# Optimization experiments

Hardware: AMD Instinct MI355X
Metric: run time of the kernel (lower is better)

Reference implementation:

```python
import jax, jax.numpy as jnp
import numpy as np
import math

# ---- constants derived from PCF.__init__(nbbins=50, sigma=0.25, npoints=1024, n_rmax=5) ----
NBBINS = 50
SIGMA = 0.25
NPOINTS = 1024
N_RMAX = 5
RMAX = float(2.0 * np.sqrt(1.0 / (2.0 * np.sqrt(3.0) * NPOINTS)))
_STEP = N_RMAX / NBBINS
RS = np.array([(i + 1) * _STEP * RMAX for i in range(NBBINS)], dtype=np.float32)
AREA = np.array([math.pi * ((r + 0.5 * RMAX) ** 2 - max(0.0, r - 0.5 * RMAX) ** 2) for r in RS],
                dtype=np.float32)
GF = float(1.0 / (np.sqrt(math.pi) * SIGMA))


def _gaussian_kernel(x):
    return GF * jnp.exp(-(x * x) / (SIGMA * SIGMA))


def _perimeter_weight(x, y, rs):
    """x, y: [N] disk centers in [0,1]^2; rs: [B]. Returns [N, B] inverse in-domain perimeter fraction."""
    full = jnp.full((x.shape[0], rs.shape[0]), 2.0 * math.pi, dtype=x.dtype)

    def corr(full_angle, dx, dy):
        # dx, dy: [N] distance to a domain edge (as in the four blocks of perimeter_weight)
        mask = rs[None, :] > dx[:, None]                       # [N, B]
        alpha = jnp.arccos(jnp.clip(dx[:, None] / rs[None, :], -1.0, 1.0))
        sub = (jnp.minimum(alpha, jnp.arctan2(dy, dx)[:, None])
               + jnp.minimum(alpha, jnp.arctan2(1.0 - dy, dx)[:, None]))
        return full_angle - jnp.where(mask, sub, 0.0)

    full = corr(full, x, y)          # left edge
    full = corr(full, 1.0 - x, y)    # right edge
    full = corr(full, y, x)          # bottom edge
    full = corr(full, 1.0 - y, x)    # top edge
    peri = jnp.clip(full / (2.0 * math.pi), 0.0, 1.0)
    pos = peri > 0
    return jnp.where(pos, 1.0 / jnp.where(pos, peri, 1.0), 0.0)


def _disk_distance(pa, pb, rmax):
    """pa: [Na,3], pb: [Nb,3] disks (x, y, r) -> pairwise disk distance [Na, Nb] (repo utils.diskDistance)."""
    diff = pa[:, None, 0:2] - pb[None, :, 0:2]
    d = jnp.sqrt(jnp.sum(diff * diff, axis=-1))                # [Na, Nb]
    ra = pa[:, 2][:, None]
    rb = pb[None, :, 2]
    r1 = jnp.maximum(ra, rb)
    r2 = jnp.minimum(ra, rb)
    extent = jnp.maximum(d + r1 + r2, 2.0 * r1)
    overlap = jnp.clip(r1 + r2 - d, 0.0, None)
    return (extent - overlap + d + r1 - r2) / rmax


def _pcf_forward(disks_a, disks_b, same_category):
    rs = jnp.asarray(RS)
    area = jnp.asarray(AREA)
    na = disks_a.shape[0]
    nb = disks_b.shape[0]
    dist = _disk_distance(disks_a, disks_b, RMAX)              # [Na, Nb]
    # val[i, j, b] = gauss(rs_b / rmax - dist_ij)
    val = _gaussian_kernel(rs[None, None, :] / RMAX - dist[:, :, None])  # [Na, Nb, B]
    if same_category:
        # exclude self-pair j == i (torch.cat of slices around i)
        eye = jnp.eye(na, nb, dtype=val.dtype)
        val = val * (1.0 - eye)[:, :, None]
    contrib = jnp.sum(val, axis=1)                             # [Na, B]
    weights = _perimeter_weight(disks_a[:, 0], disks_a[:, 1], rs)  # [Na, B] (diskfact = 1/domainLength = 1)
    density = contrib * weights / area[None, :] / nb           # [Na, B]
    pcf_mean = jnp.sum(density, axis=0) / na                   # [B]
    pcf_lower = jnp.min(density, axis=0)
    pcf_upper = jnp.max(density, axis=0)
    pcf = jnp.stack([rs / RMAX, pcf_mean], axis=1)             # [B, 2]
    return pcf, pcf_lower, pcf_upper


def setup_inputs() -> dict:
    key = jax.random.key(0)
    ka, kb = jax.random.split(key)
    disks_a = jax.random.uniform(ka, (1024, 3), dtype=jnp.float32)
    disks_b = jax.random.uniform(kb, (1024, 3), dtype=jnp.float32)
    return {"disks_a": disks_a, "disks_b": disks_b, "same_category": 0}


def reference(disks_a, disks_b, same_category):
    return _pcf_forward(disks_a, disks_b, same_category)
```

## Files before the change

### kernel.cpp

```cpp
#include <hip/hip_runtime.h>
#include <math.h>

#define NB 50

__device__ __forceinline__ float dev_rmax() {
    return (float)(2.0 * sqrt(1.0 / (2.0 * sqrt(3.0) * 1024.0)));
}

__global__ void __launch_bounds__(64)
pcf_density_kernel(const float* __restrict__ da, const float* __restrict__ db,
                   const int* __restrict__ scp, float* __restrict__ dens,
                   int na, int nb)
{
    const float RMAX = dev_rmax();
    const float inv_rmax = 1.0f / RMAX;
    const int i   = blockIdx.x;
    const int tid = threadIdx.x;
    const int sc  = scp[0];

    const float ax = da[3*i+0];
    const float ay = da[3*i+1];
    const float ar = da[3*i+2];

    float acc[NB];
#pragma unroll
    for (int b = 0; b < NB; ++b) acc[b] = 0.0f;

    for (int j = tid; j < nb; j += 64) {
        const float bx = db[3*j+0];
        const float by = db[3*j+1];
        const float br = db[3*j+2];
        const float dx = ax - bx;
        const float dy = ay - by;
        const float d  = sqrtf(dx*dx + dy*dy);
        const float r1 = fmaxf(ar, br);
        const float r2 = fminf(ar, br);
        const float extent  = fmaxf(d + r1 + r2, 2.0f*r1);
        const float overlap = fmaxf(r1 + r2 - d, 0.0f);
        const float dist = (extent - overlap + d + r1 - r2) * inv_rmax;
        const bool skip = (sc != 0) && (j == i);
        if (dist < 7.5f && !skip) {
#pragma unroll
            for (int b = 0; b < NB; ++b) {
                const float x = 0.1f * (float)(b + 1) - dist;
                acc[b] += __expf(-16.0f * x * x);
            }
        }
    }

    __shared__ float red[64 * 51];
#pragma unroll
    for (int b = 0; b < NB; ++b) red[tid * 51 + b] = acc[b];
    __syncthreads();

    if (tid < NB) {
        float s = 0.0f;
#pragma unroll 16
        for (int t = 0; t < 64; ++t) s += red[t * 51 + tid];

        const float PI = 3.14159265358979323846f;
        const float GF = 1.0f / (sqrtf(PI) * 0.25f);
        const float rs = 0.1f * (float)(tid + 1) * RMAX;

        float full = 2.0f * PI;
        const float ex[4] = { ax, 1.0f - ax, ay, 1.0f - ay };
        const float ey[4] = { ay, ay,        ax, ax        };
#pragma unroll
        for (int c = 0; c < 4; ++c) {
            if (rs > ex[c]) {
                float ratio = ex[c] / rs;
                ratio = fminf(fmaxf(ratio, -1.0f), 1.0f);
                const float alpha = acosf(ratio);
                const float a1 = atan2f(ey[c], ex[c]);
                const float a2 = atan2f(1.0f - ey[c], ex[c]);
                full -= fminf(alpha, a1) + fminf(alpha, a2);
            }
        }
        float peri = full * (1.0f / (2.0f * PI));
        peri = fminf(fmaxf(peri, 0.0f), 1.0f);
        const float w = (peri > 0.0f) ? (1.0f / peri) : 0.0f;

        const float r_out = rs + 0.5f * RMAX;
        const float r_in  = fmaxf(rs - 0.5f * RMAX, 0.0f);
        const float area  = PI * (r_out * r_out - r_in * r_in);

        const float density = (GF * s) * w / area / (float)nb;
        dens[tid * na + i] = density;
    }
}

__global__ void __launch_bounds__(64)
pcf_reduce_kernel(const float* __restrict__ dens, float* __restrict__ out, int na)
{
    const int b   = blockIdx.x;
    const int tid = threadIdx.x;
    const float RMAX = dev_rmax();

    float s = 0.0f, mn = INFINITY, mx = -INFINITY;
    for (int i = tid; i < na; i += 64) {
        const float v = dens[b * na + i];
        s  += v;
        mn  = fminf(mn, v);
        mx  = fmaxf(mx, v);
    }
#pragma unroll
    for (int off = 32; off >= 1; off >>= 1) {
        s  += __shfl_down(s, off);
        mn  = fminf(mn, __shfl_down(mn, off));
        mx  = fmaxf(mx, __shfl_down(mx, off));
    }
    if (tid == 0) {
        const float rs = 0.1f * (float)(b + 1) * RMAX;
        out[2*b + 0]  = rs / RMAX;
        out[2*b + 1]  = s / (float)na;
        out[100 + b]  = mn;
        out[150 + b]  = mx;
    }
}

extern "C" void kernel_launch(void* const* d_in, const int* in_sizes, int n_in,
                              void* d_out, int out_size, void* d_ws, size_t ws_size,
                              hipStream_t stream)
{
    const float* da = (const float*)d_in[0];
    const float* db = (const float*)d_in[1];
    const int*   sc = (const int*)d_in[2];
    float* out  = (float*)d_out;
    float* dens = (float*)d_ws;
    const int na = in_sizes[0] / 3;
    const int nb = in_sizes[1] / 3;

    pcf_density_kernel<<<na, 64, 0, stream>>>(da, db, sc, dens, na, nb);
    pcf_reduce_kernel<<<NB, 64, 0, stream>>>(dens, out, na);
}
```

Baseline: 73.14 us.

## Compact close pairs into shared list and parallelize bins across lanes

The density kernel now uses 256 threads. Each chunk of b-disks is filtered with a ballot plus prefix count into a compacted shared-memory list of close distances. Lanes then map to histogram bins and waves stride over the list, so each lane keeps one accumulator instead of 50. This removes divergence in the per-thread 50-bin loop and the register pressure of the old accumulator array, at the cost of an atomic and three barriers per chunk. The reduce kernel also moves to 256 threads with a cross-wave shared-memory reduction.

```diff
diff --git a/kernel.cpp b/kernel.cpp
--- a/kernel.cpp
+++ b/kernel.cpp
@@ -7,60 +7,80 @@
     return (float)(2.0 * sqrt(1.0 / (2.0 * sqrt(3.0) * 1024.0)));
 }
 
-__global__ void __launch_bounds__(64)
+__global__ void __launch_bounds__(256)
 pcf_density_kernel(const float* __restrict__ da, const float* __restrict__ db,
                    const int* __restrict__ scp, float* __restrict__ dens,
                    int na, int nb)
 {
     const float RMAX = dev_rmax();
     const float inv_rmax = 1.0f / RMAX;
-    const int i   = blockIdx.x;
-    const int tid = threadIdx.x;
-    const int sc  = scp[0];
+    const int i    = blockIdx.x;
+    const int tid  = threadIdx.x;
+    const int lane = tid & 63;
+    const int wave = tid >> 6;
+    const int sc   = scp[0];
+
+    __shared__ float list[256];
+    __shared__ int   cnt;
+    __shared__ float part[4 * NB];
+
+    if (tid == 0) cnt = 0;
+    __syncthreads();
 
     const float ax = da[3*i+0];
     const float ay = da[3*i+1];
     const float ar = da[3*i+2];
 
-    float acc[NB];
-#pragma unroll
-    for (int b = 0; b < NB; ++b) acc[b] = 0.0f;
+    const float binf = 0.1f * (float)(lane + 1);
+    float accb = 0.0f;
 
-    for (int j = tid; j < nb; j += 64) {
-        const float bx = db[3*j+0];
-        const float by = db[3*j+1];
-        const float br = db[3*j+2];
-        const float dx = ax - bx;
-        const float dy = ay - by;
-        const float d  = sqrtf(dx*dx + dy*dy);
-        const float r1 = fmaxf(ar, br);
-        const float r2 = fminf(ar, br);
-        const float extent  = fmaxf(d + r1 + r2, 2.0f*r1);
-        const float overlap = fmaxf(r1 + r2 - d, 0.0f);
-        const float dist = (extent - overlap + d + r1 - r2) * inv_rmax;
-        const bool skip = (sc != 0) && (j == i);
-        if (dist < 7.5f && !skip) {
-#pragma unroll
-            for (int b = 0; b < NB; ++b) {
-                const float x = 0.1f * (float)(b + 1) - dist;
-                acc[b] += __expf(-16.0f * x * x);
-            }
+    for (int base = 0; base < nb; base += 256) {
+        const int j = base + tid;
+        bool close = false;
+        float dist = 0.0f;
+        if (j < nb) {
+            const float bx = db[3*j+0];
+            const float by = db[3*j+1];
+            const float br = db[3*j+2];
+            const float dx = ax - bx;
+            const float dy = ay - by;
+            const float d  = sqrtf(dx*dx + dy*dy);
+            const float r1 = fmaxf(ar, br);
+            const float r2 = fminf(ar, br);
+            const float extent  = fmaxf(d + r1 + r2, 2.0f*r1);
+            const float overlap = fmaxf(r1 + r2 - d, 0.0f);
+            dist = (extent - overlap + d + r1 - r2) * inv_rmax;
+            close = (dist < 7.5f) && !((sc != 0) && (j == i));
         }
+        const unsigned long long m = __ballot(close);
+        const int total  = __popcll(m);
+        const int prefix = __popcll(m & ((1ull << lane) - 1ull));
+        int wbase = 0;
+        if (lane == 0) wbase = atomicAdd(&cnt, total);
+        wbase = __shfl(wbase, 0);
+        if (close) list[wbase + prefix] = dist;
+        __syncthreads();
+
+        const int M = cnt;
+        for (int k = wave; k < M; k += 4) {
+            const float dl = list[k];
+            const float x  = binf - dl;
+            accb += __expf(-16.0f * x * x);
+        }
+        __syncthreads();
+        if (tid == 0) cnt = 0;
+        __syncthreads();
     }
 
-    __shared__ float red[64 * 51];
-#pragma unroll
-    for (int b = 0; b < NB; ++b) red[tid * 51 + b] = acc[b];
+    if (lane < NB) part[wave * NB + lane] = accb;
     __syncthreads();
 
-    if (tid < NB) {
-        float s = 0.0f;
-#pragma unroll 16
-        for (int t = 0; t < 64; ++t) s += red[t * 51 + tid];
+    if (wave == 0 && lane < NB) {
+        const float s = part[lane] + part[NB + lane] + part[2*NB + lane] + part[3*NB + lane];
 
         const float PI = 3.14159265358979323846f;
         const float GF = 1.0f / (sqrtf(PI) * 0.25f);
-        const float rs = 0.1f * (float)(tid + 1) * RMAX;
+        const float rs = 0.1f * (float)(lane + 1) * RMAX;
 
         float full = 2.0f * PI;
         const float ex[4] = { ax, 1.0f - ax, ay, 1.0f - ay };
@@ -85,19 +105,23 @@
         const float area  = PI * (r_out * r_out - r_in * r_in);
 
         const float density = (GF * s) * w / area / (float)nb;
-        dens[tid * na + i] = density;
+        dens[lane * na + i] = density;
     }
 }
 
-__global__ void __launch_bounds__(64)
+__global__ void __launch_bounds__(256)
 pcf_reduce_kernel(const float* __restrict__ dens, float* __restrict__ out, int na)
 {
-    const int b   = blockIdx.x;
-    const int tid = threadIdx.x;
+    const int b    = blockIdx.x;
+    const int tid  = threadIdx.x;
+    const int lane = tid & 63;
+    const int wave = tid >> 6;
     const float RMAX = dev_rmax();
 
+    __shared__ float rs_[4], rmn[4], rmx[4];
+
     float s = 0.0f, mn = INFINITY, mx = -INFINITY;
-    for (int i = tid; i < na; i += 64) {
+    for (int i = tid; i < na; i += 256) {
         const float v = dens[b * na + i];
         s  += v;
         mn  = fminf(mn, v);
@@ -109,12 +133,17 @@
         mn  = fminf(mn, __shfl_down(mn, off));
         mx  = fmaxf(mx, __shfl_down(mx, off));
     }
+    if (lane == 0) { rs_[wave] = s; rmn[wave] = mn; rmx[wave] = mx; }
+    __syncthreads();
     if (tid == 0) {
+        float ts = rs_[0] + rs_[1] + rs_[2] + rs_[3];
+        float tmn = fminf(fminf(rmn[0], rmn[1]), fminf(rmn[2], rmn[3]));
+        float tmx = fmaxf(fmaxf(rmx[0], rmx[1]), fmaxf(rmx[2], rmx[3]));
         const float rs = 0.1f * (float)(b + 1) * RMAX;
-        out[2*b + 0]  = rs / RMAX;
-        out[2*b + 1]  = s / (float)na;
-        out[100 + b]  = mn;
-        out[150 + b]  = mx;
+        out[2*b + 0] = rs / RMAX;
+        out[2*b + 1] = ts / (float)na;
+        out[100 + b] = tmn;
+        out[150 + b] = tmx;
     }
 }
 
@@ -130,6 +159,6 @@
     const int na = in_sizes[0] / 3;
     const int nb = in_sizes[1] / 3;
 
-    pcf_density_kernel<<<na, 64, 0, stream>>>(da, db, sc, dens, na, nb);
-    pcf_reduce_kernel<<<NB, 64, 0, stream>>>(dens, out, na);
+    pcf_density_kernel<<<na, 256, 0, stream>>>(da, db, sc, dens, na, nb);
+    pcf_reduce_kernel<<<NB, 256, 0, stream>>>(dens, out, na);
 }
```

Measured after the change: 63.54 us (median of 2 runs). 13.1% less time.
